# Kernel tuning notes

Measured on AMD Instinct MI355X. Metric: run time of the kernel, lower is better.

## Reference

```python
import jax, jax.numpy as jnp
import numpy as np

ALPHA = 0.6
LOSS_WEIGHT = 1.0
BIG = 1e9


def _centered_meshgrid(M):
    # centered per-cell coordinates within an MxM block, (row, col) order
    c = jnp.arange(M, dtype=jnp.float32) - (M - 1) / 2.0
    yy, xx = jnp.meshgrid(c, c, indexing='ij')
    return jnp.stack([yy, xx], axis=-1)  # [M, M, 2]


def setup_inputs() -> dict:
    key = jax.random.key(0)
    k1, k2, k3 = jax.random.split(key, 3)
    B, H, W, M, K = 4, 64, 64, 8, 64
    pred_scores = jax.random.normal(k1, (B, H * W, K), dtype=jnp.float32)
    pred_offsets = jax.random.normal(k2, (B, H * W, K, 2), dtype=jnp.float32) * 0.5
    target = jax.random.randint(k3, (B, H * M, W * M), 0, 2, dtype=jnp.int32)
    return {"pred_scores": pred_scores, "pred_offsets": pred_offsets,
            "target": target, "H": H, "W": W, "M": M}


def _forward(pred_scores, pred_offsets, target, H, W, M):
    B = target.shape[0]
    K = pred_scores.shape[-1]
    T = M * M
    HW = H * W

    tgt = (target > 0).astype(jnp.int32)
    # [B,H,M,W,M] -> [B,H,W,M,M] -> [B,HW,T]
    tgt = tgt.reshape(B, H, M, W, M).transpose(0, 1, 3, 2, 4).reshape(B, HW, T)

    # stable descending sort of targets (positives first)
    order = jnp.argsort(-tgt, axis=-1, stable=True)          # [B,HW,T]
    block_target = jnp.take_along_axis(tgt, order, axis=-1)  # [B,HW,T]

    base_off = _centered_meshgrid(M).reshape(T, 2) / M       # [T,2]
    mask_offsets = base_off[order]                           # [B,HW,T,2]

    # broadcast cost: [B,HW,K,T]
    loc_cost = jnp.abs(pred_offsets[:, :, :, None, :] - mask_offsets[:, :, None, :, :]).sum(-1)
    cls_cost = jnp.abs(jax.nn.sigmoid(pred_scores)[..., None]
                       - block_target[:, :, None, :].astype(pred_scores.dtype))
    cost = (loc_cost ** 0.8) * (cls_cost ** 0.2) * block_target[:, :, None, :].astype(pred_scores.dtype)
    cost = jax.lax.stop_gradient(cost)  # assignment is non-differentiable

    # batched greedy assignment: for each target (in sorted order) pick the
    # cheapest not-yet-assigned prediction slot
    cost_t = jnp.moveaxis(cost, -1, 0)               # [T,B,HW,K]
    assigned0 = jnp.zeros((B, HW, K), dtype=bool)
    kidx = jnp.arange(K)

    def step(assigned, c):
        c = jnp.where(assigned, BIG, c)
        idx = jnp.argmin(c, axis=-1)                 # [B,HW]
        assigned = assigned | (kidx[None, None, :] == idx[..., None])
        return assigned, idx

    _, assign = jax.lax.scan(step, assigned0, cost_t)
    assignment = jnp.moveaxis(assign, 0, -1)          # [B,HW,T] in [0,K)

    bi = jnp.arange(B)[:, None, None]
    ni = jnp.arange(HW)[None, :, None]
    target_scores = jnp.zeros((B, HW, K), jnp.int32).at[bi, ni, assignment].set(block_target)
    target_offsets = jnp.zeros_like(pred_offsets).at[bi, ni, assignment].set(
        mask_offsets.astype(pred_offsets.dtype))

    num_pos = jnp.maximum(jnp.count_nonzero(target_scores), 1).astype(pred_scores.dtype)
    # first-call EMA: old = initial = num_pos -> normalizer = num_pos
    normalizer = num_pos

    t = target_scores.astype(pred_scores.dtype)
    p = jax.nn.sigmoid(pred_scores)
    ce = -(t * jax.nn.log_sigmoid(pred_scores) + (1.0 - t) * jax.nn.log_sigmoid(-pred_scores))
    p_t = p * t + (1.0 - p) * (1.0 - t)
    focal = ce * (1.0 - p_t) ** 2 * (ALPHA * t + (1.0 - ALPHA) * (1.0 - t))
    obj_loss = focal.sum()

    loc_loss = (jnp.abs(pred_offsets - target_offsets).sum(-1) * t).sum()

    return LOSS_WEIGHT * (obj_loss / normalizer + 10.0 * loc_loss / normalizer)


def reference(pred_scores, pred_offsets, target, H, W, M):
    return _forward(pred_scores, pred_offsets, target, H, W, M)
```

## Files before the change

kernel.cpp:

```cpp
#include <hip/hip_runtime.h>
#include <math.h>

#define HW  4096
#define KK  64
#define BLK 256
#define BPW 4

__device__ __forceinline__ unsigned umin32(unsigned a, unsigned b) { return a < b ? a : b; }

__device__ __forceinline__ float softplusf(float x) {
    return fmaxf(x, 0.0f) + log1pf(expf(-fabsf(x)));
}

__device__ __forceinline__ unsigned group_min_u32(unsigned x) {
    asm("s_nop 1\n\t"
        "v_min_u32_dpp %0, %0, %0 row_ror:1 row_mask:0xf bank_mask:0xf\n\t"
        "s_nop 1\n\t"
        "v_min_u32_dpp %0, %0, %0 row_ror:2 row_mask:0xf bank_mask:0xf\n\t"
        "s_nop 1\n\t"
        "v_min_u32_dpp %0, %0, %0 row_ror:4 row_mask:0xf bank_mask:0xf\n\t"
        "s_nop 1\n\t"
        "v_min_u32_dpp %0, %0, %0 row_ror:8 row_mask:0xf bank_mask:0xf\n\t"
        "s_nop 1"
        : "+v"(x));
    return x;
}

__global__ __launch_bounds__(BLK) void assign_loss_kernel(
    const float4* __restrict__ ps4,
    const float4* __restrict__ po4,
    const int*    __restrict__ tgt,
    float* __restrict__ pobj, float* __restrict__ ploc, int* __restrict__ pnp)
{
    const int lane = threadIdx.x & 63;
    const int wib  = threadIdx.x >> 6;
    const int wv   = blockIdx.x * 4 + wib;
    const int g    = lane >> 4;
    const int q    = lane & 15;
    const int bid  = wv * BPW + g;
    const int b    = bid >> 12;
    const int n    = bid & (HW - 1);
    const int h    = n >> 6, w = n & 63;

    const float4 sc = ps4[bid * 16 + q];
    const float4 pa = po4[bid * 32 + q * 2];
    const float4 pb = po4[bid * 32 + q * 2 + 1];
    float p0[4] = {pa.x, pa.z, pb.x, pb.z};
    float p1[4] = {pa.y, pa.w, pb.y, pb.w};
    float s [4] = {sc.x, sc.y, sc.z, sc.w};

    const int rb = (b * 512 + h * 8 + (q >> 3)) * 512 + w * 8 + (q & 7);
    int bb[4];
    #pragma unroll
    for (int v = 0; v < 4; ++v) bb[v] = tgt[rb + v * 1024] > 0;
    int cnt = bb[0] + bb[1] + bb[2] + bb[3];

    const unsigned long long B0 = __ballot(bb[0]);
    const unsigned long long B1 = __ballot(bb[1]);
    const unsigned long long B2 = __ballot(bb[2]);
    const unsigned long long B3 = __ballot(bb[3]);
    const int sh = g * 16;
    const unsigned w0 = (unsigned)(B0 >> sh) & 0xFFFFu;
    const unsigned w1 = (unsigned)(B1 >> sh) & 0xFFFFu;
    const unsigned w2 = (unsigned)(B2 >> sh) & 0xFFFFu;
    const unsigned w3 = (unsigned)(B3 >> sh) & 0xFFFFu;
    unsigned mlo = w0 | (w1 << 16);
    unsigned mhi = w2 | (w3 << 16);

    float sig[4], cl[4], locl[4];
    unsigned dead[4] = {0u, 0u, 0u, 0u};
    #pragma unroll
    for (int u = 0; u < 4; ++u) {
        sig[u]  = 1.0f / (1.0f + expf(-s[u]));
        cl[u]   = sqrtf(sqrtf(1.0f - sig[u]));
        locl[u] = 0.0f;
    }

    while (__any((mlo | mhi) != 0u)) {
        const unsigned gd = ((mlo | mhi) == 0u) ? ~0u : 0u;
        const int t = (mlo != 0u) ? (__ffs(mlo) - 1) : (31 + __ffs(mhi));
        const unsigned nhi = (mlo == 0u) ? (mhi & (mhi - 1u)) : mhi;
        mlo &= (mlo - 1u);
        mhi = nhi;

        const float by = (float)(t >> 3) * 0.125f - 0.4375f;
        const float bx = (float)(t & 7)  * 0.125f - 0.4375f;

        float l[4]; unsigned kc[4];
        #pragma unroll
        for (int u = 0; u < 4; ++u) {
            l[u]  = fabsf(p0[u] - by) + fabsf(p1[u] - bx);
            kc[u] = (__float_as_uint(l[u] * cl[u]) & ~63u) | (unsigned)(q * 4 + u);
        }
        unsigned x = umin32(umin32(kc[0] | dead[0], kc[1] | dead[1]),
                            umin32(kc[2] | dead[2], kc[3] | dead[3])) | gd;
        x = group_min_u32(x);
        #pragma unroll
        for (int u = 0; u < 4; ++u) {
            const bool win = (kc[u] == x);
            dead[u] = win ? ~0u : dead[u];
            locl[u] = win ? l[u] : locl[u];
        }
    }

    float focal = 0.0f, locs = 0.0f;
    #pragma unroll
    for (int u = 0; u < 4; ++u) {
        const bool asg = (dead[u] != 0u);
        const float ce  = asg ? softplusf(-s[u]) : softplusf(s[u]);
        const float p_t = asg ? sig[u] : (1.0f - sig[u]);
        const float om  = 1.0f - p_t;
        focal += ce * om * om * (asg ? 0.6f : 0.4f);
        locs  += locl[u];
    }

    float fc = focal, lc = locs; int cc = cnt;
    #pragma unroll
    for (int o = 32; o; o >>= 1) {
        fc += __shfl_xor(fc, o, 64);
        lc += __shfl_xor(lc, o, 64);
        cc += __shfl_xor(cc, o, 64);
    }

    __shared__ float sobj[4], sloc[4];
    __shared__ int   snp[4];
    if (lane == 0) { sobj[wib] = fc; sloc[wib] = lc; snp[wib] = cc; }
    __syncthreads();
    if (threadIdx.x == 0) {
        float o = 0.0f, l = 0.0f; int np = 0;
        #pragma unroll
        for (int u = 0; u < 4; ++u) { o += sobj[u]; l += sloc[u]; np += snp[u]; }
        pobj[blockIdx.x] = o;
        ploc[blockIdx.x] = l;
        pnp [blockIdx.x] = np;
    }
}

__global__ __launch_bounds__(256) void finalize_kernel(
    const float* __restrict__ pobj,
    const float* __restrict__ ploc,
    const int*   __restrict__ pnp,
    int nb, float* __restrict__ out)
{
    __shared__ double so[256], sl[256];
    __shared__ long long sn[256];
    double o = 0.0, l = 0.0;
    long long np = 0;
    for (int i = threadIdx.x; i < nb; i += 256) {
        o  += (double)pobj[i];
        l  += (double)ploc[i];
        np += (long long)pnp[i];
    }
    so[threadIdx.x] = o; sl[threadIdx.x] = l; sn[threadIdx.x] = np;
    __syncthreads();
    for (int st = 128; st; st >>= 1) {
        if (threadIdx.x < st) {
            so[threadIdx.x] += so[threadIdx.x + st];
            sl[threadIdx.x] += sl[threadIdx.x + st];
            sn[threadIdx.x] += sn[threadIdx.x + st];
        }
        __syncthreads();
    }
    if (threadIdx.x == 0) {
        long long npos = sn[0] > 1 ? sn[0] : 1;
        out[0] = (float)((so[0] + 10.0 * sl[0]) / (double)npos);
    }
}

extern "C" void kernel_launch(void* const* d_in, const int* in_sizes, int n_in,
                              void* d_out, int out_size, void* d_ws, size_t ws_size,
                              hipStream_t stream) {
    const float4* ps4 = (const float4*)d_in[0];
    const float4* po4 = (const float4*)d_in[1];
    const int*    tgt = (const int*)d_in[2];

    const int total_blocks = in_sizes[0] / KK;
    const int nwg = total_blocks / 16;

    float* pobj = (float*)d_ws;
    float* ploc = pobj + nwg;
    int*   pnp  = (int*)(ploc + nwg);

    assign_loss_kernel<<<nwg, BLK, 0, stream>>>(ps4, po4, tgt, pobj, ploc, pnp);
    finalize_kernel<<<1, 256, 0, stream>>>(pobj, ploc, pnp, nwg, (float*)d_out);
}
```

Baseline: 34.38 us.

## Map each block to 32 lanes with two slots per lane instead of 16×4

Changes the thread mapping so each 64-slot block is handled by 32 lanes owning two prediction slots each, rather than 16 lanes owning four. The launch doubles the number of workgroups and halves per-thread register and serial work in the greedy argmin loop. The cross-lane minimum now needs a DPP row reduction plus a ds_swizzle to combine two 16-lane rows. This costs one extra LDS-path swizzle per greedy step in exchange for more wavefronts and shorter per-step ALU chains.

```diff
diff --git a/kernel.cpp b/kernel.cpp
--- a/kernel.cpp
+++ b/kernel.cpp
@@ -4,7 +4,7 @@
 #define HW  4096
 #define KK  64
 #define BLK 256
-#define BPW 4
+#define BPW 2
 
 __device__ __forceinline__ unsigned umin32(unsigned a, unsigned b) { return a < b ? a : b; }
 
@@ -12,7 +12,7 @@
     return fmaxf(x, 0.0f) + log1pf(expf(-fabsf(x)));
 }
 
-__device__ __forceinline__ unsigned group_min_u32(unsigned x) {
+__device__ __forceinline__ unsigned row16_min_u32(unsigned x) {
     asm("s_nop 1\n\t"
         "v_min_u32_dpp %0, %0, %0 row_ror:1 row_mask:0xf bank_mask:0xf\n\t"
         "s_nop 1\n\t"
@@ -27,7 +27,7 @@
 }
 
 __global__ __launch_bounds__(BLK) void assign_loss_kernel(
-    const float4* __restrict__ ps4,
+    const float2* __restrict__ ps2,
     const float4* __restrict__ po4,
     const int*    __restrict__ tgt,
     float* __restrict__ pobj, float* __restrict__ ploc, int* __restrict__ pnp)
@@ -35,46 +35,37 @@
     const int lane = threadIdx.x & 63;
     const int wib  = threadIdx.x >> 6;
     const int wv   = blockIdx.x * 4 + wib;
-    const int g    = lane >> 4;
-    const int q    = lane & 15;
+    const int g    = lane >> 5;
+    const int q    = lane & 31;
     const int bid  = wv * BPW + g;
     const int b    = bid >> 12;
     const int n    = bid & (HW - 1);
     const int h    = n >> 6, w = n & 63;
 
-    const float4 sc = ps4[bid * 16 + q];
-    const float4 pa = po4[bid * 32 + q * 2];
-    const float4 pb = po4[bid * 32 + q * 2 + 1];
-    float p0[4] = {pa.x, pa.z, pb.x, pb.z};
-    float p1[4] = {pa.y, pa.w, pb.y, pb.w};
-    float s [4] = {sc.x, sc.y, sc.z, sc.w};
+    const float2 sc = ps2[bid * 32 + q];
+    const float4 pa = po4[bid * 32 + q];
+    const float p00 = pa.x, p01 = pa.y;
+    const float p10 = pa.z, p11 = pa.w;
+    const float s0 = sc.x, s1 = sc.y;
 
     const int rb = (b * 512 + h * 8 + (q >> 3)) * 512 + w * 8 + (q & 7);
-    int bb[4];
-    #pragma unroll
-    for (int v = 0; v < 4; ++v) bb[v] = tgt[rb + v * 1024] > 0;
-    int cnt = bb[0] + bb[1] + bb[2] + bb[3];
+    const int bb0 = tgt[rb] > 0;
+    const int bb1 = tgt[rb + 4 * 512] > 0;
+    int cnt = bb0 + bb1;
 
-    const unsigned long long B0 = __ballot(bb[0]);
-    const unsigned long long B1 = __ballot(bb[1]);
-    const unsigned long long B2 = __ballot(bb[2]);
-    const unsigned long long B3 = __ballot(bb[3]);
-    const int sh = g * 16;
-    const unsigned w0 = (unsigned)(B0 >> sh) & 0xFFFFu;
-    const unsigned w1 = (unsigned)(B1 >> sh) & 0xFFFFu;
-    const unsigned w2 = (unsigned)(B2 >> sh) & 0xFFFFu;
-    const unsigned w3 = (unsigned)(B3 >> sh) & 0xFFFFu;
-    unsigned mlo = w0 | (w1 << 16);
-    unsigned mhi = w2 | (w3 << 16);
+    const unsigned long long B0 = __ballot(bb0);
+    const unsigned long long B1 = __ballot(bb1);
+    const int sh = g * 32;
+    unsigned mlo = (unsigned)(B0 >> sh);
+    unsigned mhi = (unsigned)(B1 >> sh);
 
-    float sig[4], cl[4], locl[4];
-    unsigned dead[4] = {0u, 0u, 0u, 0u};
-    #pragma unroll
-    for (int u = 0; u < 4; ++u) {
-        sig[u]  = 1.0f / (1.0f + expf(-s[u]));
-        cl[u]   = sqrtf(sqrtf(1.0f - sig[u]));
-        locl[u] = 0.0f;
-    }
+    const float sig0 = 1.0f / (1.0f + expf(-s0));
+    const float sig1 = 1.0f / (1.0f + expf(-s1));
+    const float cl0  = sqrtf(sqrtf(1.0f - sig0));
+    const float cl1  = sqrtf(sqrtf(1.0f - sig1));
+
+    unsigned dead0 = 0u, dead1 = 0u;
+    float locl0 = 0.0f, locl1 = 0.0f;
 
     while (__any((mlo | mhi) != 0u)) {
         const unsigned gd = ((mlo | mhi) == 0u) ? ~0u : 0u;
@@ -86,32 +77,36 @@
         const float by = (float)(t >> 3) * 0.125f - 0.4375f;
         const float bx = (float)(t & 7)  * 0.125f - 0.4375f;
 
-        float l[4]; unsigned kc[4];
-        #pragma unroll
-        for (int u = 0; u < 4; ++u) {
-            l[u]  = fabsf(p0[u] - by) + fabsf(p1[u] - bx);
-            kc[u] = (__float_as_uint(l[u] * cl[u]) & ~63u) | (unsigned)(q * 4 + u);
-        }
-        unsigned x = umin32(umin32(kc[0] | dead[0], kc[1] | dead[1]),
-                            umin32(kc[2] | dead[2], kc[3] | dead[3])) | gd;
-        x = group_min_u32(x);
-        #pragma unroll
-        for (int u = 0; u < 4; ++u) {
-            const bool win = (kc[u] == x);
-            dead[u] = win ? ~0u : dead[u];
-            locl[u] = win ? l[u] : locl[u];
-        }
+        const float l0 = fabsf(p00 - by) + fabsf(p01 - bx);
+        const float l1 = fabsf(p10 - by) + fabsf(p11 - bx);
+        const unsigned k0 = (__float_as_uint(l0 * cl0) & ~63u) | (unsigned)(q * 2);
+        const unsigned k1 = (__float_as_uint(l1 * cl1) & ~63u) | (unsigned)(q * 2 + 1);
+
+        unsigned x = umin32(k0 | dead0, k1 | dead1) | gd;
+        x = row16_min_u32(x);
+        const unsigned y = (unsigned)__builtin_amdgcn_ds_swizzle((int)x, 0x401F);
+        x = umin32(x, y);
+
+        const bool w0 = (k0 == x);
+        const bool w1 = (k1 == x);
+        dead0 = w0 ? ~0u : dead0;  locl0 = w0 ? l0 : locl0;
+        dead1 = w1 ? ~0u : dead1;  locl1 = w1 ? l1 : locl1;
     }
 
     float focal = 0.0f, locs = 0.0f;
-    #pragma unroll
-    for (int u = 0; u < 4; ++u) {
-        const bool asg = (dead[u] != 0u);
-        const float ce  = asg ? softplusf(-s[u]) : softplusf(s[u]);
-        const float p_t = asg ? sig[u] : (1.0f - sig[u]);
-        const float om  = 1.0f - p_t;
-        focal += ce * om * om * (asg ? 0.6f : 0.4f);
-        locs  += locl[u];
+    {
+        const bool a0 = (dead0 != 0u);
+        const float ce0  = a0 ? softplusf(-s0) : softplusf(s0);
+        const float pt0  = a0 ? sig0 : (1.0f - sig0);
+        const float om0  = 1.0f - pt0;
+        focal += ce0 * om0 * om0 * (a0 ? 0.6f : 0.4f);
+        locs  += locl0;
+        const bool a1 = (dead1 != 0u);
+        const float ce1  = a1 ? softplusf(-s1) : softplusf(s1);
+        const float pt1  = a1 ? sig1 : (1.0f - sig1);
+        const float om1  = 1.0f - pt1;
+        focal += ce1 * om1 * om1 * (a1 ? 0.6f : 0.4f);
+        locs  += locl1;
     }
 
     float fc = focal, lc = locs; int cc = cnt;
@@ -170,17 +165,17 @@
 extern "C" void kernel_launch(void* const* d_in, const int* in_sizes, int n_in,
                               void* d_out, int out_size, void* d_ws, size_t ws_size,
                               hipStream_t stream) {
-    const float4* ps4 = (const float4*)d_in[0];
+    const float2* ps2 = (const float2*)d_in[0];
     const float4* po4 = (const float4*)d_in[1];
     const int*    tgt = (const int*)d_in[2];
 
     const int total_blocks = in_sizes[0] / KK;
-    const int nwg = total_blocks / 16;
+    const int nwg = total_blocks / 8;
 
     float* pobj = (float*)d_ws;
     float* ploc = pobj + nwg;
     int*   pnp  = (int*)(ploc + nwg);
 
-    assign_loss_kernel<<<nwg, BLK, 0, stream>>>(ps4, po4, tgt, pobj, ploc, pnp);
+    assign_loss_kernel<<<nwg, BLK, 0, stream>>>(ps2, po4, tgt, pobj, ploc, pnp);
     finalize_kernel<<<1, 256, 0, stream>>>(pobj, ploc, pnp, nwg, (float*)d_out);
 }
```

New measurement: 38.28 us. 1.11x slower.
